# Kernel optimization log

Hardware: AMD Instinct MI355X
Metric: run time of the kernel (lower is better)

The kernel has to match this reference:

```python
import jax, jax.numpy as jnp
import numpy as np

DIM = 1024
N_HEADS = 16
HEAD_DIM = DIM // N_HEADS


def setup_inputs() -> dict:
    key = jax.random.key(0)
    ks = jax.random.split(key, 6)
    s = DIM ** -0.5
    return {
        "x": jax.random.normal(ks[0], (2, 2048, DIM), dtype=jnp.float32),
        "Wq": jax.random.normal(ks[1], (DIM, DIM), dtype=jnp.float32) * s,
        "Wk": jax.random.normal(ks[2], (DIM, DIM), dtype=jnp.float32) * s,
        "Wv": jax.random.normal(ks[3], (DIM, DIM), dtype=jnp.float32) * s,
        "Wo": jax.random.normal(ks[4], (DIM, DIM), dtype=jnp.float32) * s,
        "bo": jax.random.normal(ks[5], (DIM,), dtype=jnp.float32) * 0.01,
    }


def reference(x, Wq, Wk, Wv, Wo, bo):
    B, T, C = x.shape
    H, D = N_HEADS, HEAD_DIM
    # Linear(dim, dim, bias=False): y = x @ W^T
    q = (x @ Wq.T).reshape(B, T, H, D).transpose(0, 2, 1, 3)  # B H T D
    k = (x @ Wk.T).reshape(B, T, H, D).transpose(0, 2, 1, 3)
    v = (x @ Wv.T).reshape(B, T, H, D).transpose(0, 2, 1, 3)
    q = q * (D ** -0.5)
    attn = jnp.einsum('bhqd,bhkd->bhqk', q, k)  # B H T T
    causal_mask = jnp.triu(jnp.ones((T, T), dtype=bool), k=1)
    attn = jnp.where(causal_mask, -jnp.inf, attn)
    attn = jax.nn.softmax(attn, axis=-1)
    out = jnp.einsum('bhqk,bhkd->bhqd', attn, v)  # B H T D
    out = out.transpose(0, 2, 1, 3).reshape(B, T, C)
    return out @ Wo.T + bo
```

## Files before the change

kernel.cpp:

```cpp
#include <hip/hip_runtime.h>
#include <math.h>

typedef __attribute__((ext_vector_type(8))) short bf16x8;
typedef __attribute__((ext_vector_type(4))) float f32x4;
typedef __attribute__((ext_vector_type(16))) float f32x16;

__device__ __forceinline__ ushort f2bf(float f) {
  union { float f; unsigned u; } v; v.f = f;
  return (ushort)((v.u + 0x8000u) >> 16);
}

__device__ __forceinline__ void g2l16(const void* g, void* l) {
  __builtin_amdgcn_global_load_lds((const __attribute__((address_space(1))) unsigned*)g,
                                   (__attribute__((address_space(3))) unsigned*)l, 16, 0, 0);
}

__global__ __launch_bounds__(256) void cast_all(const float* __restrict__ x,
                                                const float* __restrict__ Wq,
                                                const float* __restrict__ Wk,
                                                const float* __restrict__ Wv,
                                                const float* __restrict__ Wo,
                                                ushort* __restrict__ xbf,
                                                ushort* __restrict__ wcat,
                                                float4* __restrict__ O32) {
  int i = blockIdx.x * 256 + threadIdx.x;
  if (i < 1048576) {
    float4 v = ((const float4*)x)[i];
    ushort4 u; u.x = f2bf(v.x); u.y = f2bf(v.y); u.z = f2bf(v.z); u.w = f2bf(v.w);
    ((ushort4*)xbf)[i] = u;
  } else if (i < 2097152) {
    int j = i - 1048576;
    int sel = j >> 18;
    const float* src = (sel == 0) ? Wq : (sel == 1) ? Wk : (sel == 2) ? Wv : Wo;
    float scale = (sel == 0) ? 0.125f * 1.44269504088896f : 1.0f;
    float4 v = ((const float4*)src)[j & 0x3FFFF];
    ushort4 u;
    u.x = f2bf(v.x * scale); u.y = f2bf(v.y * scale);
    u.z = f2bf(v.z * scale); u.w = f2bf(v.w * scale);
    ((ushort4*)wcat)[j] = u;
  } else {
    O32[i - 2097152] = float4{0.f, 0.f, 0.f, 0.f};
  }
}

__global__ __launch_bounds__(256) void gemm_qkv(const ushort* __restrict__ A,
                                                const ushort* __restrict__ B,
                                                ushort* __restrict__ C3,
                                                ushort* __restrict__ Vt) {
  const int K = 1024;
  __shared__ __align__(16) ushort smem[17408];
  ushort* As = smem;
  ushort* Bs = smem + 8192;
  const int m0 = blockIdx.y * 128, n0 = blockIdx.x * 128;
  const int tid = threadIdx.x, lane = tid & 63, wid = tid >> 6;
  const int quad = lane >> 4, lc = lane & 15;
  const int lrow = lane >> 2, lcol = (lane & 3) * 8;
  const int wm = (wid >> 1) * 64, wn = (wid & 1) * 64;

  f32x4 acc[4][4] = {};

  auto stage = [&](int k0, int nb) {
    const ushort* Ag = A + (size_t)(m0 + wid * 32 + lrow) * K + k0 + lcol;
    g2l16(Ag, &As[nb * 4096 + wid * 1024]);
    g2l16(Ag + (size_t)16 * K, &As[nb * 4096 + wid * 1024 + 512]);
    const ushort* Bg = B + (size_t)(n0 + wid * 32 + lrow) * K + k0 + lcol;
    g2l16(Bg, &Bs[nb * 4096 + wid * 1024]);
    g2l16(Bg + (size_t)16 * K, &Bs[nb * 4096 + wid * 1024 + 512]);
  };

  stage(0, 0);
  for (int k0 = 0; k0 < K; k0 += 32) {
    const int nb = (k0 >> 5) & 1;
    __syncthreads();
    if (k0 + 32 < K) stage(k0 + 32, nb ^ 1);

    bf16x8 af[4], bfr[4];
#pragma unroll
    for (int t = 0; t < 4; t++)
      af[t] = *(const bf16x8*)&As[nb * 4096 + (wm + t * 16 + lc) * 32 + quad * 8];
#pragma unroll
    for (int t = 0; t < 4; t++)
      bfr[t] = *(const bf16x8*)&Bs[nb * 4096 + (wn + t * 16 + lc) * 32 + quad * 8];
#pragma unroll
    for (int mt = 0; mt < 4; mt++)
#pragma unroll
      for (int nt = 0; nt < 4; nt++)
        acc[mt][nt] = __builtin_amdgcn_mfma_f32_16x16x32_bf16(af[mt], bfr[nt], acc[mt][nt], 0, 0, 0);
  }

  const int sel = n0 >> 10;
  if (sel < 2) {
#pragma unroll
    for (int mt = 0; mt < 4; mt++) {
#pragma unroll
      for (int r = 0; r < 4; r++) {
        int row = m0 + wm + mt * 16 + quad * 4 + r;
#pragma unroll
        for (int nt = 0; nt < 4; nt++) {
          int col = n0 + wn + nt * 16 + lc;
          size_t dst = ((size_t)sel << 22) + (size_t)row * 1024 + (col & 1023);
          C3[dst] = f2bf(acc[mt][nt][r]);
        }
      }
    }
  } else {
    __syncthreads();
#pragma unroll
    for (int mt = 0; mt < 4; mt++)
#pragma unroll
      for (int r = 0; r < 4; r++) {
        int tl = wm + mt * 16 + quad * 4 + r;
#pragma unroll
        for (int nt = 0; nt < 4; nt++)
          smem[(wn + nt * 16 + lc) * 136 + tl] = f2bf(acc[mt][nt][r]);
      }
    __syncthreads();
    const int hd0 = n0 - 2048, b = m0 >> 11, t_base = m0 & 2047;
#pragma unroll
    for (int i = 0; i < 8; i++) {
      int idx = i * 256 + tid;
      int dl = idx >> 4, tc = (idx & 15) * 8;
      uint4 v = *(const uint4*)&smem[dl * 136 + tc];
      int hd = hd0 + dl;
      *(uint4*)(Vt + (size_t)(b * 16 + (hd >> 6)) * 131072 +
                (size_t)(hd & 63) * 2048 + t_base + tc) = v;
    }
  }
}

__global__ __launch_bounds__(256) void gemm_proj(const ushort* __restrict__ A,
                                                 const ushort* __restrict__ B,
                                                 float* __restrict__ C,
                                                 const float* __restrict__ bias) {
  const int K = 1024;
  __shared__ __align__(16) ushort As[2][2][128 * 32];
  __shared__ __align__(16) ushort Bs[2][2][64 * 32];
  const int m0 = blockIdx.y * 128, n0 = blockIdx.x * 64;
  const int tid = threadIdx.x, lane = tid & 63, wid = tid >> 6;
  const int quad = lane >> 4, lc = lane & 15;
  const int lrow = lane >> 2, lcol = (lane & 3) * 8;
  const int wm = (wid >> 1) * 64, wn = (wid & 1) * 32;

  f32x4 acc[4][2] = {};

  auto stage = [&](int k0, int nb) {
    const ushort* Ag = A + (size_t)(m0 + wid * 32 + lrow) * K + k0 + lcol;
    g2l16(Ag,                       &As[nb][0][wid * 1024]);
    g2l16(Ag + (size_t)16 * K,      &As[nb][0][wid * 1024 + 512]);
    g2l16(Ag + 32,                  &As[nb][1][wid * 1024]);
    g2l16(Ag + (size_t)16 * K + 32, &As[nb][1][wid * 1024 + 512]);
    const ushort* Bg = B + (size_t)(n0 + wid * 16 + lrow) * K + k0 + lcol;
    g2l16(Bg,      &Bs[nb][0][wid * 512]);
    g2l16(Bg + 32, &Bs[nb][1][wid * 512]);
  };

  stage(0, 0);
  for (int k0 = 0; k0 < K; k0 += 64) {
    const int nb = (k0 >> 6) & 1;
    __syncthreads();
    if (k0 + 64 < K) stage(k0 + 64, nb ^ 1);

#pragma unroll
    for (int ks = 0; ks < 2; ks++) {
      bf16x8 af[4], bfr[2];
#pragma unroll
      for (int t = 0; t < 4; t++)
        af[t] = *(const bf16x8*)&As[nb][ks][(wm + t * 16 + lc) * 32 + quad * 8];
#pragma unroll
      for (int t = 0; t < 2; t++)
        bfr[t] = *(const bf16x8*)&Bs[nb][ks][(wn + t * 16 + lc) * 32 + quad * 8];
#pragma unroll
      for (int mt = 0; mt < 4; mt++)
#pragma unroll
        for (int nt = 0; nt < 2; nt++)
          acc[mt][nt] = __builtin_amdgcn_mfma_f32_16x16x32_bf16(af[mt], bfr[nt], acc[mt][nt], 0, 0, 0);
    }
  }

#pragma unroll
  for (int mt = 0; mt < 4; mt++) {
#pragma unroll
    for (int r = 0; r < 4; r++) {
      int row = m0 + wm + mt * 16 + quad * 4 + r;
#pragma unroll
      for (int nt = 0; nt < 2; nt++) {
        int col = n0 + wn + nt * 16 + lc;
        C[(size_t)row * 1024 + col] = acc[mt][nt][r] + bias[col];
      }
    }
  }
}

__global__ __launch_bounds__(128, 5) void attn_kernel(const ushort* __restrict__ Qb,
                                                      const ushort* __restrict__ Kb,
                                                      const ushort* __restrict__ Vt,
                                                      float* __restrict__ O32,
                                                      float* __restrict__ L32) {
  __shared__ __align__(16) ushort Ks[4096];
  __shared__ __align__(16) ushort Vs[4096];

  const int bh = blockIdx.x, b = bh >> 4, h = bh & 15;
  int rem = (int)blockIdx.y, qi2 = 31;
  while (true) { int c = (qi2 + 8) >> 3; if (rem < c) break; rem -= c; qi2--; }
  const int ci = rem;
  const int t0 = ci * 8;
  const int t1 = min(t0 + 8, qi2 + 1);

  const int tid = threadIdx.x, lane = tid & 63, wid = tid >> 6;
  const int hi = lane >> 5, ln = lane & 31;
  const int qbw = qi2 * 64 + wid * 32;
  const int qg = qbw + ln;

  const size_t kbase = (size_t)(b * 2048) * 1024 + h * 64;
  const size_t vbase = (size_t)bh * 131072;

  bf16x8 qf[4];
  {
    const ushort* Qp = Qb + kbase + (size_t)qg * 1024 + hi * 8;
#pragma unroll
    for (int dc = 0; dc < 4; dc++)
      qf[dc] = *(const bf16x8*)(Qp + dc * 16);
  }

  f32x16 o_acc[2] = {};
  float l_own = 0.f;

  const int krow = lane >> 3, kcol = lane & 7;
  const int dsw = (kcol ^ krow) << 3;

  auto stage = [&](int kb) {
    if (wid == 0) {
      const ushort* gK = Kb + kbase + (size_t)(kb + krow) * 1024 + dsw;
#pragma unroll
      for (int i = 0; i < 8; i++)
        g2l16(gK + (size_t)(i * 8) * 1024, &Ks[i * 512]);
    } else {
      const ushort* gV = Vt + vbase + (size_t)krow * 2048 + kb + dsw;
#pragma unroll
      for (int i = 0; i < 8; i++)
        g2l16(gV + (size_t)(i * 8) * 2048, &Vs[i * 512]);
    }
  };

  const int sx = ln & 7;

  for (int kt = t0; kt < t1; kt++) {
    const int kb = kt * 64;
    __builtin_amdgcn_s_barrier();
    stage(kb);
    asm volatile("s_waitcnt vmcnt(0)" ::: "memory");
    __builtin_amdgcn_s_barrier();

#pragma unroll
    for (int g64 = 0; g64 < 2; g64++) {
      if (kb + g64 * 32 > qbw + 31) continue;
      f32x16 s;
#pragma unroll
      for (int z = 0; z < 16; z++) s[z] = 0.f;
      __builtin_amdgcn_s_setprio(1);
#pragma unroll
      for (int dc = 0; dc < 4; dc++) {
        bf16x8 kf = *(const bf16x8*)&Ks[(g64 * 32 + ln) * 64 + (((dc * 2 + hi) ^ sx) << 3)];
        s = __builtin_amdgcn_mfma_f32_32x32x16_bf16(kf, qf[dc], s, 0, 0, 0);
      }
      __builtin_amdgcn_s_setprio(0);

      unsigned U[8];
      const bool dmask = (kb + g64 * 32 + 31 > qbw);
      if (dmask) {
        const int c = qg - kb - g64 * 32 - hi * 4;
#pragma unroll
        for (int g = 0; g < 4; g++) {
          float e[4];
#pragma unroll
          for (int j = 0; j < 4; j++) {
            float sv = s[g * 4 + j];
            if (g * 8 + j > c) sv = -1e30f;
            e[j] = __builtin_amdgcn_exp2f(sv);
          }
          l_own += (e[0] + e[1]) + (e[2] + e[3]);
          union { float f; unsigned u; } f0{e[0]}, f1{e[1]}, f2{e[2]}, f3{e[3]};
          U[g * 2]     = __builtin_amdgcn_perm(f1.u + 0x8000u, f0.u + 0x8000u, 0x07060302u);
          U[g * 2 + 1] = __builtin_amdgcn_perm(f3.u + 0x8000u, f2.u + 0x8000u, 0x07060302u);
        }
      } else {
#pragma unroll
        for (int g = 0; g < 4; g++) {
          float e[4];
#pragma unroll
          for (int j = 0; j < 4; j++)
            e[j] = __builtin_amdgcn_exp2f(s[g * 4 + j]);
          l_own += (e[0] + e[1]) + (e[2] + e[3]);
          union { float f; unsigned u; } f0{e[0]}, f1{e[1]}, f2{e[2]}, f3{e[3]};
          U[g * 2]     = __builtin_amdgcn_perm(f1.u + 0x8000u, f0.u + 0x8000u, 0x07060302u);
          U[g * 2 + 1] = __builtin_amdgcn_perm(f3.u + 0x8000u, f2.u + 0x8000u, 0x07060302u);
        }
      }

      __builtin_amdgcn_s_setprio(1);
#pragma unroll
      for (int half = 0; half < 2; half++) {
        const int m = g64 * 2 + half;
        bf16x8 pfrag;
#pragma unroll
        for (int w = 0; w < 4; w++) ((unsigned*)&pfrag)[w] = U[half * 4 + w];
#pragma unroll
        for (int dg = 0; dg < 2; dg++) {
          const ushort* vrow = &Vs[(dg * 32 + ln) * 64];
          bf16x8 vbf;
          *(unsigned long long*)&vbf =
              *(const unsigned long long*)&vrow[(((2 * m) ^ sx) << 3) + 4 * hi];
          *((unsigned long long*)&vbf + 1) =
              *(const unsigned long long*)&vrow[(((2 * m + 1) ^ sx) << 3) + 4 * hi];
          o_acc[dg] = __builtin_amdgcn_mfma_f32_32x32x16_bf16(pfrag, vbf, o_acc[dg], 0, 0, 0);
        }
      }
      __builtin_amdgcn_s_setprio(0);
    }
  }

  {
    float lt = l_own + __shfl_xor(l_own, 32);
    if (hi == 0) atomicAdd(&L32[(size_t)bh * 2048 + qg], lt);
  }
#pragma unroll
  for (int r = 0; r < 16; r++) {
    int q = qbw + (r & 3) + ((r >> 2) << 3) + hi * 4;
    size_t orow = ((size_t)(b * 2048) + q) * 1024 + h * 64 + ln;
    atomicAdd(&O32[orow], o_acc[0][r]);
    atomicAdd(&O32[orow + 32], o_acc[1][r]);
  }
}

__global__ __launch_bounds__(256) void normalize_kernel(const float* __restrict__ O32,
                                                        const float* __restrict__ L32,
                                                        ushort* __restrict__ Out) {
  const int row = blockIdx.x;
  const int tid = threadIdx.x;
  const int col = tid * 4;
  const int b = row >> 11, t = row & 2047, h = col >> 6;
  const float inv = 1.0f / L32[(size_t)(b * 16 + h) * 2048 + t];
  float4 o = ((const float4*)(O32 + (size_t)row * 1024))[tid];
  ushort4 u;
  u.x = f2bf(o.x * inv); u.y = f2bf(o.y * inv);
  u.z = f2bf(o.z * inv); u.w = f2bf(o.w * inv);
  ((ushort4*)(Out + (size_t)row * 1024))[tid] = u;
}

extern "C" void kernel_launch(void* const* d_in, const int* in_sizes, int n_in,
                              void* d_out, int out_size, void* d_ws, size_t ws_size,
                              hipStream_t stream) {
  const float* x  = (const float*)d_in[0];
  const float* Wq = (const float*)d_in[1];
  const float* Wk = (const float*)d_in[2];
  const float* Wv = (const float*)d_in[3];
  const float* Wo = (const float*)d_in[4];
  const float* bo = (const float*)d_in[5];
  float* out = (float*)d_out;

  char* ws = (char*)d_ws;
  ushort* xbf  = (ushort*)(ws);
  ushort* wcat = (ushort*)(ws + (8ull  << 20));
  ushort* qkv  = (ushort*)(ws + (16ull << 20));
  ushort* Qp   = qkv;
  ushort* Kp   = qkv + (1ull << 22);
  ushort* Vt   = qkv + (2ull << 22);
  float*  L32  = (float*)ws;
  float*  O32  = out;
  ushort* attn_out = Qp;

  cast_all<<<12288, 256, 0, stream>>>(x, Wq, Wk, Wv, Wo, xbf, wcat, (float4*)O32);

  gemm_qkv<<<dim3(24, 32), 256, 0, stream>>>(xbf, wcat, qkv, Vt);

  hipMemsetAsync(L32, 0, (size_t)32 * 2048 * 4, stream);

  attn_kernel<<<dim3(32, 80), 128, 0, stream>>>(Qp, Kp, Vt, O32, L32);

  normalize_kernel<<<4096, 256, 0, stream>>>(O32, L32, attn_out);

  gemm_proj<<<dim3(16, 32), 256, 0, stream>>>(
      attn_out, wcat + (size_t)3072 * 1024, out, bo);
}
```

Before: 203.4 us.

## Load K and V fragments directly from global memory, dropping LDS staging

The attention kernel no longer stages K and V tiles into shared memory with barriers. Each wave now reads its K and V MFMA fragments straight from global memory, relying on the L1/L2 caches. This removes the LDS traffic and both block barriers per key tile. In exchange it adds redundant global loads across the two waves, and the V reads become 8-byte strided accesses, so load latency is no longer hidden by the staging.

Result: slower. 266.0 us (+30.8%).

```diff
diff --git a/kernel.cpp b/kernel.cpp
--- a/kernel.cpp
+++ b/kernel.cpp
@@ -196,9 +196,6 @@
                                                       const ushort* __restrict__ Vt,
                                                       float* __restrict__ O32,
                                                       float* __restrict__ L32) {
-  __shared__ __align__(16) ushort Ks[4096];
-  __shared__ __align__(16) ushort Vs[4096];
-
   const int bh = blockIdx.x, b = bh >> 4, h = bh & 15;
   int rem = (int)blockIdx.y, qi2 = 31;
   while (true) { int c = (qi2 + 8) >> 3; if (rem < c) break; rem -= c; qi2--; }
@@ -225,31 +222,11 @@
   f32x16 o_acc[2] = {};
   float l_own = 0.f;
 
-  const int krow = lane >> 3, kcol = lane & 7;
-  const int dsw = (kcol ^ krow) << 3;
-
-  auto stage = [&](int kb) {
-    if (wid == 0) {
-      const ushort* gK = Kb + kbase + (size_t)(kb + krow) * 1024 + dsw;
-#pragma unroll
-      for (int i = 0; i < 8; i++)
-        g2l16(gK + (size_t)(i * 8) * 1024, &Ks[i * 512]);
-    } else {
-      const ushort* gV = Vt + vbase + (size_t)krow * 2048 + kb + dsw;
-#pragma unroll
-      for (int i = 0; i < 8; i++)
-        g2l16(gV + (size_t)(i * 8) * 2048, &Vs[i * 512]);
-    }
-  };
-
-  const int sx = ln & 7;
+  const ushort* Kp = Kb + kbase;
+  const ushort* Vp = Vt + vbase;
 
   for (int kt = t0; kt < t1; kt++) {
     const int kb = kt * 64;
-    __builtin_amdgcn_s_barrier();
-    stage(kb);
-    asm volatile("s_waitcnt vmcnt(0)" ::: "memory");
-    __builtin_amdgcn_s_barrier();
 
 #pragma unroll
     for (int g64 = 0; g64 < 2; g64++) {
@@ -257,10 +234,11 @@
       f32x16 s;
 #pragma unroll
       for (int z = 0; z < 16; z++) s[z] = 0.f;
+      const ushort* krow = Kp + (size_t)(kb + g64 * 32 + ln) * 1024 + hi * 8;
       __builtin_amdgcn_s_setprio(1);
 #pragma unroll
       for (int dc = 0; dc < 4; dc++) {
-        bf16x8 kf = *(const bf16x8*)&Ks[(g64 * 32 + ln) * 64 + (((dc * 2 + hi) ^ sx) << 3)];
+        bf16x8 kf = *(const bf16x8*)(krow + dc * 16);
         s = __builtin_amdgcn_mfma_f32_32x32x16_bf16(kf, qf[dc], s, 0, 0, 0);
       }
       __builtin_amdgcn_s_setprio(0);
@@ -306,12 +284,10 @@
         for (int w = 0; w < 4; w++) ((unsigned*)&pfrag)[w] = U[half * 4 + w];
 #pragma unroll
         for (int dg = 0; dg < 2; dg++) {
-          const ushort* vrow = &Vs[(dg * 32 + ln) * 64];
+          const ushort* vr = Vp + (size_t)(dg * 32 + ln) * 2048 + kb + 16 * m + 4 * hi;
           bf16x8 vbf;
-          *(unsigned long long*)&vbf =
-              *(const unsigned long long*)&vrow[(((2 * m) ^ sx) << 3) + 4 * hi];
-          *((unsigned long long*)&vbf + 1) =
-              *(const unsigned long long*)&vrow[(((2 * m + 1) ^ sx) << 3) + 4 * hi];
+          *(unsigned long long*)&vbf = *(const unsigned long long*)vr;
+          *((unsigned long long*)&vbf + 1) = *(const unsigned long long*)(vr + 8);
           o_acc[dg] = __builtin_amdgcn_mfma_f32_32x32x16_bf16(pfrag, vbf, o_acc[dg], 0, 0, 0);
         }
       }
```

## Prefetch next K/V tile into registers while computing current tile in attention

Applied to the files above, without the earlier changes.

Replaces the synchronous global-to-LDS staging with register prefetch. The next 64-key K/V tile is loaded into registers before computing on the current tile, then written to LDS after a barrier, so global load latency overlaps the MFMA work. Occupancy hint is lowered from 5 to 3 waves per SIMD to make room for the extra registers that hold the prefetched tile. The cost is higher register pressure and an extra barrier per iteration, and fewer resident waves may hide less latency elsewhere.

Result: faster. 192.2 us (-5.5%).

```diff
diff --git a/kernel.cpp b/kernel.cpp
--- a/kernel.cpp
+++ b/kernel.cpp
@@ -191,7 +191,7 @@
   }
 }
 
-__global__ __launch_bounds__(128, 5) void attn_kernel(const ushort* __restrict__ Qb,
+__global__ __launch_bounds__(128, 3) void attn_kernel(const ushort* __restrict__ Qb,
                                                       const ushort* __restrict__ Kb,
                                                       const ushort* __restrict__ Vt,
                                                       float* __restrict__ O32,
@@ -227,29 +227,41 @@
 
   const int krow = lane >> 3, kcol = lane & 7;
   const int dsw = (kcol ^ krow) << 3;
-
-  auto stage = [&](int kb) {
-    if (wid == 0) {
-      const ushort* gK = Kb + kbase + (size_t)(kb + krow) * 1024 + dsw;
-#pragma unroll
-      for (int i = 0; i < 8; i++)
-        g2l16(gK + (size_t)(i * 8) * 1024, &Ks[i * 512]);
-    } else {
-      const ushort* gV = Vt + vbase + (size_t)krow * 2048 + kb + dsw;
-#pragma unroll
-      for (int i = 0; i < 8; i++)
-        g2l16(gV + (size_t)(i * 8) * 2048, &Vs[i * 512]);
-    }
-  };
+  const bool isK = (wid == 0);
+  const ushort* gsrc0 = isK ? (Kb + kbase + (size_t)krow * 1024 + dsw)
+                            : (Vt + vbase + (size_t)krow * 2048 + dsw);
+  const size_t rstride = isK ? (size_t)8 * 1024 : (size_t)8 * 2048;
+  const size_t tmul = isK ? (size_t)1024 : (size_t)1;
+  ushort* ldst = isK ? Ks : Vs;
+
+  uint4 rg0, rg1, rg2, rg3, rg4, rg5, rg6, rg7;
+#define ATTN_ISSUE(KB) do { \
+    const ushort* gp_ = gsrc0 + (size_t)(KB) * tmul; \
+    rg0 = *(const uint4*)(gp_);                rg1 = *(const uint4*)(gp_ + rstride); \
+    rg2 = *(const uint4*)(gp_ + 2 * rstride);  rg3 = *(const uint4*)(gp_ + 3 * rstride); \
+    rg4 = *(const uint4*)(gp_ + 4 * rstride);  rg5 = *(const uint4*)(gp_ + 5 * rstride); \
+    rg6 = *(const uint4*)(gp_ + 6 * rstride);  rg7 = *(const uint4*)(gp_ + 7 * rstride); \
+  } while (0)
+#define ATTN_COMMIT() do { \
+    ushort* dp_ = ldst + lane * 8; \
+    *(uint4*)(dp_)        = rg0;  *(uint4*)(dp_ + 512)  = rg1; \
+    *(uint4*)(dp_ + 1024) = rg2;  *(uint4*)(dp_ + 1536) = rg3; \
+    *(uint4*)(dp_ + 2048) = rg4;  *(uint4*)(dp_ + 2560) = rg5; \
+    *(uint4*)(dp_ + 3072) = rg6;  *(uint4*)(dp_ + 3584) = rg7; \
+  } while (0)
 
   const int sx = ln & 7;
+
+  ATTN_ISSUE(t0 * 64);
+  ATTN_COMMIT();
+  __syncthreads();
 
   for (int kt = t0; kt < t1; kt++) {
     const int kb = kt * 64;
-    __builtin_amdgcn_s_barrier();
-    stage(kb);
-    asm volatile("s_waitcnt vmcnt(0)" ::: "memory");
-    __builtin_amdgcn_s_barrier();
+    if (kt + 1 < t1) {
+      ATTN_ISSUE(kb + 64);
+      __builtin_amdgcn_sched_barrier(0);
+    }
 
 #pragma unroll
     for (int g64 = 0; g64 < 2; g64++) {
@@ -317,7 +329,15 @@
       }
       __builtin_amdgcn_s_setprio(0);
     }
-  }
+
+    __syncthreads();
+    if (kt + 1 < t1) {
+      ATTN_COMMIT();
+      __syncthreads();
+    }
+  }
+#undef ATTN_ISSUE
+#undef ATTN_COMMIT
 
   {
     float lt = l_own + __shfl_xor(l_own, 32);
```

## Process 64 query rows per wave in attention to reuse K/V tiles

Applied to the files above, without the earlier changes.

Each wave now handles two 32-row query sub-blocks instead of one, so every K fragment and V fragment loaded from LDS feeds two MFMAs. The block tile grows to 128 queries, the grid is halved to 40 y-blocks with a new closed-form chunk mapping, and the launch-bounds occupancy hint drops from 5 to 2 to make room for the doubled accumulators. The aim is to halve LDS and global K/V traffic per query. The cost is higher register pressure, lower occupancy and fewer blocks, which may worsen load balance across the causal triangle.

New measurement: 202.4 us. No clear change (-0.5%).

```diff
diff --git a/kernel.cpp b/kernel.cpp
--- a/kernel.cpp
+++ b/kernel.cpp
@@ -191,7 +191,7 @@
   }
 }
 
-__global__ __launch_bounds__(128, 5) void attn_kernel(const ushort* __restrict__ Qb,
+__global__ __launch_bounds__(128, 2) void attn_kernel(const ushort* __restrict__ Qb,
                                                       const ushort* __restrict__ Kb,
                                                       const ushort* __restrict__ Vt,
                                                       float* __restrict__ O32,
@@ -200,30 +200,33 @@
   __shared__ __align__(16) ushort Vs[4096];
 
   const int bh = blockIdx.x, b = bh >> 4, h = bh & 15;
-  int rem = (int)blockIdx.y, qi2 = 31;
-  while (true) { int c = (qi2 + 8) >> 3; if (rem < c) break; rem -= c; qi2--; }
-  const int ci = rem;
+  const int f = (int)blockIdx.y;
+  int qi, ci;
+  if (f < 16)      { qi = 12 + (f >> 2); ci = f & 3; }
+  else if (f < 28) { int g = f - 16; int q3 = g / 3; qi = 8 + q3; ci = g - 3 * q3; }
+  else if (f < 36) { int g = f - 28; qi = 4 + (g >> 1); ci = g & 1; }
+  else             { qi = f - 36; ci = 0; }
   const int t0 = ci * 8;
-  const int t1 = min(t0 + 8, qi2 + 1);
+  const int t1 = min(t0 + 8, 2 * qi + 2);
 
   const int tid = threadIdx.x, lane = tid & 63, wid = tid >> 6;
   const int hi = lane >> 5, ln = lane & 31;
-  const int qbw = qi2 * 64 + wid * 32;
-  const int qg = qbw + ln;
+  const int qbw = qi * 128 + wid * 64;
 
   const size_t kbase = (size_t)(b * 2048) * 1024 + h * 64;
   const size_t vbase = (size_t)bh * 131072;
 
-  bf16x8 qf[4];
-  {
-    const ushort* Qp = Qb + kbase + (size_t)qg * 1024 + hi * 8;
+  bf16x8 qf[2][4];
+#pragma unroll
+  for (int qs = 0; qs < 2; qs++) {
+    const ushort* Qp = Qb + kbase + (size_t)(qbw + qs * 32 + ln) * 1024 + hi * 8;
 #pragma unroll
     for (int dc = 0; dc < 4; dc++)
-      qf[dc] = *(const bf16x8*)(Qp + dc * 16);
-  }
-
-  f32x16 o_acc[2] = {};
-  float l_own = 0.f;
+      qf[qs][dc] = *(const bf16x8*)(Qp + dc * 16);
+  }
+
+  f32x16 o_acc[2][2] = {};
+  float l_own[2] = {0.f, 0.f};
 
   const int krow = lane >> 3, kcol = lane & 7;
   const int dsw = (kcol ^ krow) << 3;
@@ -246,64 +249,76 @@
 
   for (int kt = t0; kt < t1; kt++) {
     const int kb = kt * 64;
-    __builtin_amdgcn_s_barrier();
+    __syncthreads();
     stage(kb);
-    asm volatile("s_waitcnt vmcnt(0)" ::: "memory");
-    __builtin_amdgcn_s_barrier();
+    __syncthreads();
 
 #pragma unroll
     for (int g64 = 0; g64 < 2; g64++) {
-      if (kb + g64 * 32 > qbw + 31) continue;
-      f32x16 s;
-#pragma unroll
-      for (int z = 0; z < 16; z++) s[z] = 0.f;
-      __builtin_amdgcn_s_setprio(1);
-#pragma unroll
-      for (int dc = 0; dc < 4; dc++) {
-        bf16x8 kf = *(const bf16x8*)&Ks[(g64 * 32 + ln) * 64 + (((dc * 2 + hi) ^ sx) << 3)];
-        s = __builtin_amdgcn_mfma_f32_32x32x16_bf16(kf, qf[dc], s, 0, 0, 0);
-      }
-      __builtin_amdgcn_s_setprio(0);
-
-      unsigned U[8];
-      const bool dmask = (kb + g64 * 32 + 31 > qbw);
-      if (dmask) {
-        const int c = qg - kb - g64 * 32 - hi * 4;
-#pragma unroll
-        for (int g = 0; g < 4; g++) {
-          float e[4];
-#pragma unroll
-          for (int j = 0; j < 4; j++) {
-            float sv = s[g * 4 + j];
-            if (g * 8 + j > c) sv = -1e30f;
-            e[j] = __builtin_amdgcn_exp2f(sv);
+      if (kb + g64 * 32 > qbw + 63) continue;
+      const bool skip0 = (kb + g64 * 32 > qbw + 31);
+
+      bf16x8 kf[4];
+#pragma unroll
+      for (int dc = 0; dc < 4; dc++)
+        kf[dc] = *(const bf16x8*)&Ks[(g64 * 32 + ln) * 64 + (((dc * 2 + hi) ^ sx) << 3)];
+
+      unsigned pa[2][2][4];
+#pragma unroll
+      for (int qs = 0; qs < 2; qs++) {
+        if (qs == 0 && skip0) continue;
+        const int qb2 = qbw + qs * 32;
+        f32x16 s;
+#pragma unroll
+        for (int z = 0; z < 16; z++) s[z] = 0.f;
+        __builtin_amdgcn_s_setprio(1);
+#pragma unroll
+        for (int dc = 0; dc < 4; dc++)
+          s = __builtin_amdgcn_mfma_f32_32x32x16_bf16(kf[dc], qf[qs][dc], s, 0, 0, 0);
+        __builtin_amdgcn_s_setprio(0);
+
+        unsigned U[8];
+        const bool dmask = (kb + g64 * 32 + 31 > qb2);
+        if (dmask) {
+          const int c = qb2 + ln - kb - g64 * 32 - hi * 4;
+#pragma unroll
+          for (int g = 0; g < 4; g++) {
+            float e[4];
+#pragma unroll
+            for (int j = 0; j < 4; j++) {
+              float sv = s[g * 4 + j];
+              if (g * 8 + j > c) sv = -1e30f;
+              e[j] = __builtin_amdgcn_exp2f(sv);
+            }
+            l_own[qs] += (e[0] + e[1]) + (e[2] + e[3]);
+            union { float f; unsigned u; } f0{e[0]}, f1{e[1]}, f2{e[2]}, f3{e[3]};
+            U[g * 2]     = __builtin_amdgcn_perm(f1.u + 0x8000u, f0.u + 0x8000u, 0x07060302u);
+            U[g * 2 + 1] = __builtin_amdgcn_perm(f3.u + 0x8000u, f2.u + 0x8000u, 0x07060302u);
           }
-          l_own += (e[0] + e[1]) + (e[2] + e[3]);
-          union { float f; unsigned u; } f0{e[0]}, f1{e[1]}, f2{e[2]}, f3{e[3]};
-          U[g * 2]     = __builtin_amdgcn_perm(f1.u + 0x8000u, f0.u + 0x8000u, 0x07060302u);
-          U[g * 2 + 1] = __builtin_amdgcn_perm(f3.u + 0x8000u, f2.u + 0x8000u, 0x07060302u);
+        } else {
+#pragma unroll
+          for (int g = 0; g < 4; g++) {
+            float e[4];
+#pragma unroll
+            for (int j = 0; j < 4; j++)
+              e[j] = __builtin_amdgcn_exp2f(s[g * 4 + j]);
+            l_own[qs] += (e[0] + e[1]) + (e[2] + e[3]);
+            union { float f; unsigned u; } f0{e[0]}, f1{e[1]}, f2{e[2]}, f3{e[3]};
+            U[g * 2]     = __builtin_amdgcn_perm(f1.u + 0x8000u, f0.u + 0x8000u, 0x07060302u);
+            U[g * 2 + 1] = __builtin_amdgcn_perm(f3.u + 0x8000u, f2.u + 0x8000u, 0x07060302u);
+          }
         }
-      } else {
-#pragma unroll
-        for (int g = 0; g < 4; g++) {
-          float e[4];
-#pragma unroll
-          for (int j = 0; j < 4; j++)
-            e[j] = __builtin_amdgcn_exp2f(s[g * 4 + j]);
-          l_own += (e[0] + e[1]) + (e[2] + e[3]);
-          union { float f; unsigned u; } f0{e[0]}, f1{e[1]}, f2{e[2]}, f3{e[3]};
-          U[g * 2]     = __builtin_amdgcn_perm(f1.u + 0x8000u, f0.u + 0x8000u, 0x07060302u);
-          U[g * 2 + 1] = __builtin_amdgcn_perm(f3.u + 0x8000u, f2.u + 0x8000u, 0x07060302u);
-        }
+#pragma unroll
+        for (int half = 0; half < 2; half++)
+#pragma unroll
+          for (int w = 0; w < 4; w++)
+            pa[qs][half][w] = U[half * 4 + w];
       }
 
       __builtin_amdgcn_s_setprio(1);
 #pragma unroll
       for (int half = 0; half < 2; half++) {
         const int m = g64 * 2 + half;
-        bf16x8 pfrag;
-#pragma unroll
-        for (int w = 0; w < 4; w++) ((unsigned*)&pfrag)[w] = U[half * 4 + w];
 #pragma unroll
         for (int dg = 0; dg < 2; dg++) {
           const ushort* vrow = &Vs[(dg * 32 + ln) * 64];
@@ -312,23 +327,31 @@
               *(const unsigned long long*)&vrow[(((2 * m) ^ sx) << 3) + 4 * hi];
           *((unsigned long long*)&vbf + 1) =
               *(const unsigned long long*)&vrow[(((2 * m + 1) ^ sx) << 3) + 4 * hi];
-          o_acc[dg] = __builtin_amdgcn_mfma_f32_32x32x16_bf16(pfrag, vbf, o_acc[dg], 0, 0, 0);
+#pragma unroll
+          for (int qs = 0; qs < 2; qs++) {
+            if (qs == 0 && skip0) continue;
+            bf16x8 pfrag;
+#pragma unroll
+            for (int w = 0; w < 4; w++) ((unsigned*)&pfrag)[w] = pa[qs][half][w];
+            o_acc[qs][dg] = __builtin_amdgcn_mfma_f32_32x32x16_bf16(pfrag, vbf, o_acc[qs][dg], 0, 0, 0);
+          }
         }
       }
       __builtin_amdgcn_s_setprio(0);
     }
   }
 
-  {
-    float lt = l_own + __shfl_xor(l_own, 32);
-    if (hi == 0) atomicAdd(&L32[(size_t)bh * 2048 + qg], lt);
-  }
-#pragma unroll
-  for (int r = 0; r < 16; r++) {
-    int q = qbw + (r & 3) + ((r >> 2) << 3) + hi * 4;
-    size_t orow = ((size_t)(b * 2048) + q) * 1024 + h * 64 + ln;
-    atomicAdd(&O32[orow], o_acc[0][r]);
-    atomicAdd(&O32[orow + 32], o_acc[1][r]);
+#pragma unroll
+  for (int qs = 0; qs < 2; qs++) {
+    float lt = l_own[qs] + __shfl_xor(l_own[qs], 32);
+    if (hi == 0) atomicAdd(&L32[(size_t)bh * 2048 + qbw + qs * 32 + ln], lt);
+#pragma unroll
+    for (int r = 0; r < 16; r++) {
+      int q = qbw + qs * 32 + (r & 3) + ((r >> 2) << 3) + hi * 4;
+      size_t orow = ((size_t)(b * 2048) + q) * 1024 + h * 64 + ln;
+      atomicAdd(&O32[orow], o_acc[qs][0][r]);
+      atomicAdd(&O32[orow + 32], o_acc[qs][1][r]);
+    }
   }
 }
 
@@ -375,7 +398,7 @@
 
   hipMemsetAsync(L32, 0, (size_t)32 * 2048 * 4, stream);
 
-  attn_kernel<<<dim3(32, 80), 128, 0, stream>>>(Qp, Kp, Vt, O32, L32);
+  attn_kernel<<<dim3(32, 40), 128, 0, stream>>>(Qp, Kp, Vt, O32, L32);
 
   normalize_kernel<<<4096, 256, 0, stream>>>(O32, L32, attn_out);
 
```
